# Optimization experiments

Measured on AMD Instinct MI355X. Metric: run time of the kernel, lower is better.

Reference implementation:

```python
import jax, jax.numpy as jnp
import numpy as np

NUM_EMBED = 1024
EMBED_DIM = 64
BETA = 0.25
DECAY = 0.99


def setup_inputs() -> dict:
    key = jax.random.key(0)
    k1, k2 = jax.random.split(key, 2)
    z = jax.random.normal(k1, (16, EMBED_DIM, 64, 64), dtype=jnp.float32)
    embedding = jax.random.uniform(
        k2, (NUM_EMBED, EMBED_DIM), dtype=jnp.float32,
        minval=-1.0 / NUM_EMBED, maxval=1.0 / NUM_EMBED)
    embed_prob = jnp.zeros((NUM_EMBED,), dtype=jnp.float32)
    return {"z": z, "embedding": embedding, "embed_prob": embed_prob}


def reference(z, embedding, embed_prob):
    # Training-mode forward of VectorQuantiser (anchor='closest', not yet init).
    b, c, h, w = z.shape
    zc = jnp.transpose(z, (0, 2, 3, 1))              # b h w c
    zf = zc.reshape(-1, c)                           # [N, d]
    zsg = jax.lax.stop_gradient(zf)

    # d = -||z||^2 - ||e||^2 + 2 z.e  (negative squared L2 distance), [N, K]
    d = (-jnp.sum(zsg * zsg, axis=1, keepdims=True)
         - jnp.sum(embedding * embedding, axis=1)
         + 2.0 * jnp.einsum('nd,kd->nk', zsg, embedding))

    # indices[:, -1] after ascending sort == argmax along codebook axis
    idx = jnp.argmax(d, axis=1)                      # [N]

    # one-hot @ weight == gather
    z_q = jnp.take(embedding, idx, axis=0).reshape(zc.shape)  # b h w c

    loss = (BETA * jnp.mean((jax.lax.stop_gradient(z_q) - zc) ** 2)
            + jnp.mean((z_q - jax.lax.stop_gradient(zc)) ** 2))

    # straight-through estimator
    z_q_st = zc + jax.lax.stop_gradient(z_q - zc)
    z_q_out = jnp.transpose(z_q_st, (0, 3, 1, 2))    # b c h w

    n = zf.shape[0]
    # avg_probs = mean of one-hot encodings over tokens == histogram / N
    avg_probs = jnp.zeros((NUM_EMBED,), dtype=z.dtype).at[idx].add(1.0) / n
    perplexity = jnp.exp(-jnp.sum(avg_probs * jnp.log(avg_probs + 1e-10)))

    embed_prob_new = embed_prob * DECAY + (1.0 - DECAY) * avg_probs

    # anchor='closest': per-codeword, pick the z with largest d (smallest distance)
    closest = jnp.argmax(d, axis=0)                  # [K]
    random_feat = zsg[closest]                       # [K, d]
    decay = jnp.exp(-(embed_prob_new * NUM_EMBED * 10.0) / (1.0 - DECAY)
                    - 1e-3)[:, None]                 # [K, 1]
    new_embedding = embedding * (1.0 - decay) + random_feat * decay

    encoding_indices = idx.reshape(b, h, w)
    return (z_q_out, loss, perplexity, new_embedding, embed_prob_new,
            encoding_indices)
```

## Files before the change

### kernel.cpp

```cpp
#include <hip/hip_runtime.h>


#define MARGIN 2e-4f
#define CERT   2e-4f

#define WS_ROW   0
#define WS_COL   524288
#define WS_CNT   532480
#define WS_LOSS  536576
#define WS_EN2   536592
#define WS_LCNT  540688
#define WS_ZN2   541696
#define WS_EBH   803840
#define WS_EBL   934912
#define WS_LIST  1065984
#define WS_CBM   1328128
#define WS_BYTES 3425280
#define WS_ZERO  540720

typedef __attribute__((ext_vector_type(8))) short short8v;
typedef __attribute__((ext_vector_type(4))) float f32x4;

__device__ __forceinline__ unsigned int f32_ord(float x) {
    unsigned int b = __float_as_uint(x);
    return (b & 0x80000000u) ? ~b : (b | 0x80000000u);
}
__device__ __forceinline__ float ord_f32(unsigned int u) {
    unsigned int b = (u & 0x80000000u) ? (u & 0x7FFFFFFFu) : ~u;
    return __uint_as_float(b);
}

__device__ __forceinline__ unsigned short f2bf(float f) {
    unsigned int u = __float_as_uint(f);
    return (unsigned short)((u + 0x7FFFu + ((u >> 16) & 1u)) >> 16);
}
__device__ __forceinline__ float bf2f(unsigned short h) {
    return __uint_as_float((unsigned int)h << 16);
}

template <typename F>
__device__ __forceinline__ float np_pairwise64_sq(F get) {
    float r[8];
#pragma unroll
    for (int j = 0; j < 8; ++j) {
        float v = get(j);
        r[j] = __fmul_rn(v, v);
    }
#pragma unroll
    for (int i = 8; i < 64; i += 8) {
#pragma unroll
        for (int j = 0; j < 8; ++j) {
            float v = get(i + j);
            r[j] = __fadd_rn(r[j], __fmul_rn(v, v));
        }
    }
    return __fadd_rn(__fadd_rn(__fadd_rn(r[0], r[1]), __fadd_rn(r[2], r[3])),
                     __fadd_rn(__fadd_rn(r[4], r[5]), __fadd_rn(r[6], r[7])));
}

__global__ __launch_bounds__(256) void k_prep(
    const float* __restrict__ emb, float* __restrict__ en2,
    unsigned int* __restrict__ ebh32, unsigned int* __restrict__ ebl32) {
    const int t = threadIdx.x;
    const int k = blockIdx.x * 256 + t;
    const float* a = emb + (size_t)k * 64;
    float ar[64];
#pragma unroll
    for (int i = 0; i < 64; ++i) ar[i] = a[i];
    en2[k] = np_pairwise64_sq([&](int i) { return ar[i]; });
#pragma unroll
    for (int wd = 0; wd < 32; ++wd) {
        float e0 = ar[2 * wd], e1 = ar[2 * wd + 1];
        unsigned short h0 = f2bf(e0), h1 = f2bf(e1);
        ebh32[k * 32 + wd] = (unsigned int)h0 | ((unsigned int)h1 << 16);
        unsigned short l0 = f2bf(__fsub_rn(e0, bf2f(h0)));
        unsigned short l1 = f2bf(__fsub_rn(e1, bf2f(h1)));
        ebl32[k * 32 + wd] = (unsigned int)l0 | ((unsigned int)l1 << 16);
    }
}

__global__ __launch_bounds__(512, 2) void k_mfma(
    const float* __restrict__ z,
    const unsigned short* __restrict__ ebh, const unsigned short* __restrict__ ebl,
    float* __restrict__ zn2, const float* __restrict__ en2,
    float* __restrict__ cbm, unsigned long long* __restrict__ wsrow,
    unsigned int* __restrict__ lcnt, unsigned int* __restrict__ list) {
    const int t = threadIdx.x, l = t & 63, w = t >> 6;
    const int n0 = blockIdx.x * 128;
    const int tw = n0 + w * 16;
    const int lm = l & 15, kg = l >> 4;
    const int b   = n0 >> 12;
    const int hw0 = n0 & 4095;

    __shared__ __align__(16) unsigned char smem[45056];
    unsigned int* eh   = (unsigned int*)(smem);
    unsigned int* el   = (unsigned int*)(smem + 18432);
    float*        en2l = (float*)(smem + 36864);
    unsigned int* cmU  = (unsigned int*)(smem + 40960);
    float*        zl   = (float*)(smem);
    float*        zntmp= (float*)(smem + 36864);
    int*          bcnt  = (int*)(smem);
    unsigned int* bbase = (unsigned int*)(smem + 4);
    unsigned int* blist = (unsigned int*)(smem + 8);

    const float* zsrc = z + (size_t)b * 262144 + hw0;
#pragma unroll
    for (int it = 0; it < 16; ++it) {
        int idx = it * 512 + t;
        int c = idx >> 7, tok = idx & 127;
        zl[c * 129 + tok] = zsrc[(size_t)c * 4096 + tok];
    }
    __syncthreads();

    if (t < 128) {
        float v = np_pairwise64_sq([&](int i) { return zl[i * 129 + t]; });
        zn2[n0 + t] = v;
        zntmp[t] = v;
    }
    const int tokA = w * 16 + lm;
    short8v ah0, ah1, al0, al1;
#pragma unroll
    for (int j = 0; j < 8; ++j) {
        float z0 = zl[(kg * 8 + j) * 129 + tokA];
        float z1 = zl[(32 + kg * 8 + j) * 129 + tokA];
        unsigned short h0 = f2bf(z0);
        unsigned short h1 = f2bf(z1);
        ah0[j] = (short)h0;
        ah1[j] = (short)h1;
        al0[j] = (short)f2bf(__fsub_rn(z0, bf2f(h0)));
        al1[j] = (short)f2bf(__fsub_rn(z1, bf2f(h1)));
    }
    __syncthreads();

    float nzn2[4];
#pragma unroll
    for (int j = 0; j < 4; ++j) nzn2[j] = -zntmp[w * 16 + kg * 4 + j];
    __syncthreads();

    for (int i = t; i < 1024; i += 512) { en2l[i] = en2[i]; cmU[i] = 0u; }
    const uint4* EH4 = reinterpret_cast<const uint4*>(ebh);
    const uint4* EL4 = reinterpret_cast<const uint4*>(ebl);
    const int scode = t >> 3;
    const int sword = (t & 7) ^ (scode & 7);
    const int swd   = sword * 4;
    const int sidx  = scode * 8 + sword;
    {
        uint4 hv = EH4[sidx], lv = EL4[sidx];
        *reinterpret_cast<uint4*>(&eh[0 * 2304 + scode * 36 + swd]) = hv;
        *reinterpret_cast<uint4*>(&el[0 * 2304 + scode * 36 + swd]) = lv;
    }

    float v1[4] = {-3.4e38f, -3.4e38f, -3.4e38f, -3.4e38f};
    float v2[4] = {-3.4e38f, -3.4e38f, -3.4e38f, -3.4e38f};
    int   c1[4] = {0, 0, 0, 0};

    __syncthreads();

    for (int g = 0; g < 16; ++g) {
        const int buf = g & 1;
        const bool pf = (g < 15);
        uint4 hv, lv;
        if (pf) {
            hv = EH4[(g + 1) * 512 + sidx];
            lv = EL4[(g + 1) * 512 + sidx];
        }

#pragma unroll
        for (int sc = 0; sc < 4; ++sc) {
            const int cl = sc * 16 + lm;
            const short8v bh0 = *reinterpret_cast<const short8v*>(&eh[buf * 2304 + cl * 36 + kg * 4]);
            const short8v bh1 = *reinterpret_cast<const short8v*>(&eh[buf * 2304 + cl * 36 + 16 + kg * 4]);
            const short8v bl0 = *reinterpret_cast<const short8v*>(&el[buf * 2304 + cl * 36 + kg * 4]);
            const short8v bl1 = *reinterpret_cast<const short8v*>(&el[buf * 2304 + cl * 36 + 16 + kg * 4]);

            f32x4 a1 = {0.f, 0.f, 0.f, 0.f};
            f32x4 a2 = {0.f, 0.f, 0.f, 0.f};
            __builtin_amdgcn_s_setprio(1);
            a1 = __builtin_amdgcn_mfma_f32_16x16x32_bf16(ah0, bh0, a1, 0, 0, 0);
            a1 = __builtin_amdgcn_mfma_f32_16x16x32_bf16(ah1, bh1, a1, 0, 0, 0);
            a2 = __builtin_amdgcn_mfma_f32_16x16x32_bf16(ah0, bl0, a2, 0, 0, 0);
            a2 = __builtin_amdgcn_mfma_f32_16x16x32_bf16(ah1, bl1, a2, 0, 0, 0);
            a2 = __builtin_amdgcn_mfma_f32_16x16x32_bf16(al0, bh0, a2, 0, 0, 0);
            a2 = __builtin_amdgcn_mfma_f32_16x16x32_bf16(al1, bh1, a2, 0, 0, 0);
            __builtin_amdgcn_s_setprio(0);

            const int code = g * 64 + cl;
            const float en2v = en2l[code];
            float cm = -3.4e38f;
#pragma unroll
            for (int j = 0; j < 4; ++j) {
                float acc  = __fadd_rn(a1[j], a2[j]);
                float base = __fsub_rn(nzn2[j], en2v);
                float s    = fmaf(2.0f, acc, base);
                bool gt = s > v1[j];
                v2[j] = fmaxf(fminf(s, v1[j]), v2[j]);
                v1[j] = fmaxf(v1[j], s);
                c1[j] = gt ? code : c1[j];
                cm = fmaxf(cm, s);
            }
            cm = fmaxf(cm, __shfl_xor(cm, 16, 64));
            cm = fmaxf(cm, __shfl_xor(cm, 32, 64));
            if (l < 16) atomicMax(&cmU[code], f32_ord(cm));
        }

        if (pf) {
            *reinterpret_cast<uint4*>(&eh[(buf ^ 1) * 2304 + scode * 36 + swd]) = hv;
            *reinterpret_cast<uint4*>(&el[(buf ^ 1) * 2304 + scode * 36 + swd]) = lv;
        }
        __syncthreads();
    }

    if (t == 0) *bcnt = 0;
    __syncthreads();
#pragma unroll
    for (int j = 0; j < 4; ++j) {
        unsigned long long key =
            ((unsigned long long)f32_ord(v1[j]) << 32) |
            (unsigned long long)(unsigned int)(~(unsigned int)c1[j]);
        float w2 = v2[j];
#pragma unroll
        for (int m = 1; m < 16; m <<= 1) {
            unsigned long long ok = __shfl_xor(key, m, 64);
            float ov2 = __shfl_xor(w2, m, 64);
            unsigned long long lk = (key < ok) ? key : ok;
            float lv2 = ord_f32((unsigned int)(lk >> 32));
            w2 = fmaxf(fmaxf(w2, ov2), lv2);
            key = (key > ok) ? key : ok;
        }
        if (lm == 0) {
            const int tn = tw + kg * 4 + j;
            float v1m = ord_f32((unsigned int)(key >> 32));
            if (__fsub_rn(v1m, w2) > CERT) {
                wsrow[tn] = key;
            } else {
                int p = atomicAdd(bcnt, 1);
                blist[p] = (unsigned int)tn;
            }
        }
    }
    __syncthreads();
    if (t == 0 && *bcnt > 0) *bbase = atomicAdd(lcnt, (unsigned int)*bcnt);
    __syncthreads();
    {
        const int cb2 = *bcnt;
        for (int i = t; i < cb2; i += 512) list[*bbase + i] = blist[i];
    }

    for (int code = t; code < 1024; code += 512)
        cbm[(size_t)code * 512 + blockIdx.x] = ord_f32(cmU[code]);
}

__global__ __launch_bounds__(256) void k_rescore(
    const float* __restrict__ z, const float* __restrict__ emb,
    const float* __restrict__ zn2, const float* __restrict__ en2,
    const float* __restrict__ cbm,
    const unsigned int* __restrict__ list, const unsigned int* __restrict__ lcnt,
    unsigned long long* __restrict__ wscol,
    unsigned long long* __restrict__ wsrow) {
    const int t = threadIdx.x;
    if (blockIdx.x < 1024) {
        const int k = blockIdx.x;
        __shared__ float red[256];
        __shared__ int   hlist[512];
        __shared__ int   hcnt;
        float a  = cbm[(size_t)k * 512 + t];
        float b2 = cbm[(size_t)k * 512 + 256 + t];
        red[t] = fmaxf(a, b2);
        if (t == 0) hcnt = 0;
        __syncthreads();
        for (int st = 128; st; st >>= 1) {
            if (t < st) red[t] = fmaxf(red[t], red[t + st]);
            __syncthreads();
        }
        const float thr = red[0] - MARGIN;
        if (a >= thr)  { int p = atomicAdd(&hcnt, 1); hlist[p] = t; }
        if (b2 >= thr) { int p = atomicAdd(&hcnt, 1); hlist[p] = t + 256; }
        __syncthreads();
        const int hc = hcnt;
        const float en2k = en2[k];
        const float4* ek = reinterpret_cast<const float4*>(emb + (size_t)k * 64);

        for (int h = 0; h < hc; ++h) {
            const int g = hlist[h];
            if (t < 128) {
                const int n = g * 128 + t;
                const int b = n >> 12, hw = n & 4095;
                const float* zp = z + (size_t)b * 262144 + hw;
                float c0 = 0.f, c1 = 0.f, c2 = 0.f, c3 = 0.f;
#pragma unroll
                for (int j = 0; j < 16; ++j) {
                    float4 e = ek[j];
                    c0 = fmaf(e.x, zp[(size_t)(4 * j + 0) * 4096], c0);
                    c1 = fmaf(e.y, zp[(size_t)(4 * j + 1) * 4096], c1);
                    c2 = fmaf(e.z, zp[(size_t)(4 * j + 2) * 4096], c2);
                    c3 = fmaf(e.w, zp[(size_t)(4 * j + 3) * 4096], c3);
                }
                float dot = (c0 + c1) + (c2 + c3);
                float d = __fadd_rn(__fsub_rn(-zn2[n], en2k), 2.0f * dot);
                unsigned long long key =
                    ((unsigned long long)f32_ord(d) << 32) |
                    (unsigned long long)(unsigned int)(~(unsigned int)n);
#pragma unroll
                for (int m = 1; m < 64; m <<= 1) {
                    unsigned long long o = __shfl_xor(key, m, 64);
                    if (o > key) key = o;
                }
                if ((t & 63) == 0) atomicMax(&wscol[k], key);
            }
        }
    } else {
        const int bid2 = blockIdx.x - 1024;
        const int k0 = (bid2 & 63) * 16;
        const int xs = bid2 >> 6;
        const unsigned int cnt = *lcnt;
        const float4* E4 = reinterpret_cast<const float4*>(emb);
        for (unsigned int i = (unsigned int)xs * 256 + t; i < cnt;
             i += 64 * 256) {
            const int n = (int)list[i];
            const int b = n >> 12, hw = n & 4095;
            const float* zp = z + (size_t)b * 262144 + hw;
            const float nz = -zn2[n];
            unsigned long long best = 0ull;
            for (int kk = 0; kk < 16; ++kk) {
                const int k = k0 + kk;
                const float4* ek = E4 + (size_t)k * 16;
                float c0 = 0.f, c1 = 0.f, c2 = 0.f, c3 = 0.f;
#pragma unroll
                for (int j = 0; j < 16; ++j) {
                    float4 e = ek[j];
                    c0 = fmaf(e.x, zp[(size_t)(4 * j + 0) * 4096], c0);
                    c1 = fmaf(e.y, zp[(size_t)(4 * j + 1) * 4096], c1);
                    c2 = fmaf(e.z, zp[(size_t)(4 * j + 2) * 4096], c2);
                    c3 = fmaf(e.w, zp[(size_t)(4 * j + 3) * 4096], c3);
                }
                float dot = (c0 + c1) + (c2 + c3);
                float d = __fadd_rn(__fsub_rn(nz, en2[k]), 2.0f * dot);
                unsigned long long key =
                    ((unsigned long long)f32_ord(d) << 32) |
                    (unsigned long long)(unsigned int)(~(unsigned int)k);
                if (key > best) best = key;
            }
            atomicMax(&wsrow[n], best);
        }
    }
}

__global__ __launch_bounds__(256) void k_tokens(
    const float* __restrict__ z, const float* __restrict__ emb,
    const unsigned long long* __restrict__ wsrow,
    unsigned int* __restrict__ counts, double* __restrict__ loss_acc,
    float* __restrict__ out_zq, float* __restrict__ out_idx) {
    const int t    = threadIdx.x;
    const int lane = t & 63;
    const int q    = t >> 6;
    const int n    = blockIdx.x * 64 + lane;
    const int b    = n >> 12;
    const int hw   = n & 4095;

    unsigned long long key = wsrow[n];
    int idx = (int)(~(unsigned int)(key & 0xFFFFFFFFull));
    if (q == 0) {
        out_idx[n] = (float)idx;
        atomicAdd(&counts[idx], 1u);
    }

    const float* zp = z + (size_t)b * 262144 + hw;
    float*       op = out_zq + (size_t)b * 262144 + hw;
    const float* ep = emb + (size_t)idx * 64;

    double ls = 0.0;
#pragma unroll
    for (int c = q * 16; c < q * 16 + 16; ++c) {
        float zc   = zp[(size_t)c * 4096];
        float eq   = ep[c];
        float diff = __fsub_rn(eq, zc);
        float sq   = __fmul_rn(diff, diff);
        ls += (double)sq;
        op[(size_t)c * 4096] = __fadd_rn(zc, diff);
    }

    __shared__ double sred[256];
    sred[q * 64 + lane] = ls;
    __syncthreads();
    if (t < 64) {
        sred[t] = (sred[t] + sred[64 + t]) + (sred[128 + t] + sred[192 + t]);
    }
    __syncthreads();
    for (int st = 32; st; st >>= 1) {
        if (t < st) sred[t] += sred[t + st];
        __syncthreads();
    }
    if (t == 0) atomicAdd(loss_acc, sred[0]);
}

__global__ __launch_bounds__(1024) void k_tail(
    const float* __restrict__ z, const float* __restrict__ emb,
    const float* __restrict__ embed_prob,
    const unsigned long long* __restrict__ wscol,
    const unsigned int* __restrict__ counts,
    const double* __restrict__ loss_acc,
    float* __restrict__ out_newemb, float* __restrict__ out_loss,
    float* __restrict__ out_perp, float* __restrict__ out_prob) {
    const int k = blockIdx.x * 16 + (threadIdx.x >> 6);
    const int c = threadIdx.x & 63;

    float avg  = (float)counts[k] * (1.0f / 65536.0f);
    float pnew = __fadd_rn(__fmul_rn(embed_prob[k], 0.99f),
                           __fmul_rn(0.01f, avg));
    float tt = __fdiv_rn(__fmul_rn(__fmul_rn(pnew, 1024.0f), 10.0f), 0.01f);
    float dk = expf(__fsub_rn(-tt, 1e-3f));
    float omd = __fsub_rn(1.0f, dk);

    unsigned long long ck = wscol[k];
    int cn  = (int)(~(unsigned int)(ck & 0xFFFFFFFFull));
    int cb  = cn >> 12;
    int chw = cn & 4095;

    float rf = z[(size_t)cb * 262144 + (size_t)c * 4096 + chw];
    float e  = emb[(size_t)k * 64 + c];
    out_newemb[(size_t)k * 64 + c] =
        __fadd_rn(__fmul_rn(e, omd), __fmul_rn(rf, dk));

    if (blockIdx.x == 0) {
        const int q = threadIdx.x;

        float avg2  = (float)counts[q] * (1.0f / 65536.0f);
        float pnew2 = __fadd_rn(__fmul_rn(embed_prob[q], 0.99f),
                                __fmul_rn(0.01f, avg2));
        out_prob[q] = pnew2;

        float term = __fmul_rn(avg2, logf(__fadd_rn(avg2, 1e-10f)));
        __shared__ double red[1024];
        red[q] = (double)term;
        __syncthreads();
        for (int st = 512; st; st >>= 1) {
            if (q < st) red[q] += red[q + st];
            __syncthreads();
        }
        if (q == 0) {
            float s32 = (float)red[0];
            out_perp[0] = expf(-s32);
            double lm = loss_acc[0] / 4194304.0;
            float  m  = (float)lm;
            out_loss[0] = __fadd_rn(__fmul_rn(0.25f, m), m);
        }
    }
}

extern "C" void kernel_launch(void* const* d_in, const int* in_sizes, int n_in,
                              void* d_out, int out_size, void* d_ws, size_t ws_size,
                              hipStream_t stream) {
    const float* z    = (const float*)d_in[0];
    const float* emb  = (const float*)d_in[1];
    const float* prob = (const float*)d_in[2];

    float* out        = (float*)d_out;
    float* out_zq     = out;
    float* out_loss   = out + 4194304;
    float* out_perp   = out + 4194305;
    float* out_newemb = out + 4194306;
    float* out_prob   = out + 4259842;
    float* out_idx    = out + 4260866;

    char* ws = (char*)d_ws;
    unsigned long long* wsrow = (unsigned long long*)(ws + WS_ROW);
    unsigned long long* wscol = (unsigned long long*)(ws + WS_COL);
    unsigned int*       cnts  = (unsigned int*)(ws + WS_CNT);
    double*             lacc  = (double*)(ws + WS_LOSS);
    float*              en2   = (float*)(ws + WS_EN2);
    unsigned int*       lcnt  = (unsigned int*)(ws + WS_LCNT);
    float*              zn2   = (float*)(ws + WS_ZN2);
    unsigned short*     ebh   = (unsigned short*)(ws + WS_EBH);
    unsigned short*     ebl   = (unsigned short*)(ws + WS_EBL);
    unsigned int*       list  = (unsigned int*)(ws + WS_LIST);
    float*              cbm   = (float*)(ws + WS_CBM);

    hipMemsetAsync(d_ws, 0, WS_ZERO, stream);

    hipLaunchKernelGGL(k_prep, dim3(4), dim3(256), 0, stream,
                       emb, en2, (unsigned int*)ebh, (unsigned int*)ebl);
    hipLaunchKernelGGL(k_mfma, dim3(512), dim3(512), 0, stream,
                       z, ebh, ebl, zn2, en2, cbm, wsrow, lcnt, list);
    hipLaunchKernelGGL(k_rescore, dim3(5120), dim3(256), 0, stream,
                       z, emb, zn2, en2, cbm, list, lcnt, wscol, wsrow);
    hipLaunchKernelGGL(k_tokens, dim3(1024), dim3(256), 0, stream,
                       z, emb, wsrow, cnts, lacc, out_zq, out_idx);
    hipLaunchKernelGGL(k_tail, dim3(64), dim3(1024), 0, stream,
                       z, emb, prob, wscol, cnts, lacc,
                       out_newemb, out_loss, out_perp, out_prob);
}
```

Before: 206.2 us.

## Fold workspace zeroing into prep kernel, split MFMA chains, vectorize codeword loads

Removes the separate hipMemsetAsync and has a fifth block of k_prep zero only the column, loss and list-count workspace regions. Rows that go to rescoring now get wsrow explicitly written to zero, since that region is no longer cleared. The six MFMAs are regrouped into three independent accumulator chains to shorten dependency stalls, and k_tokens loads each codeword slice with float4 vector loads. The extra accumulator adds a float add and changes summation order slightly, and correctness now depends on every workspace region that needs zeroing actually being covered.

```diff
diff --git a/kernel.cpp b/kernel.cpp
--- a/kernel.cpp
+++ b/kernel.cpp
@@ -16,7 +16,6 @@
 #define WS_LIST  1065984
 #define WS_CBM   1328128
 #define WS_BYTES 3425280
-#define WS_ZERO  540720
 
 typedef __attribute__((ext_vector_type(8))) short short8v;
 typedef __attribute__((ext_vector_type(4))) float f32x4;
@@ -60,22 +59,30 @@
 
 __global__ __launch_bounds__(256) void k_prep(
     const float* __restrict__ emb, float* __restrict__ en2,
-    unsigned int* __restrict__ ebh32, unsigned int* __restrict__ ebl32) {
+    unsigned int* __restrict__ ebh32, unsigned int* __restrict__ ebl32,
+    unsigned int* __restrict__ wszero ) {
     const int t = threadIdx.x;
-    const int k = blockIdx.x * 256 + t;
-    const float* a = emb + (size_t)k * 64;
-    float ar[64];
-#pragma unroll
-    for (int i = 0; i < 64; ++i) ar[i] = a[i];
-    en2[k] = np_pairwise64_sq([&](int i) { return ar[i]; });
-#pragma unroll
-    for (int wd = 0; wd < 32; ++wd) {
-        float e0 = ar[2 * wd], e1 = ar[2 * wd + 1];
-        unsigned short h0 = f2bf(e0), h1 = f2bf(e1);
-        ebh32[k * 32 + wd] = (unsigned int)h0 | ((unsigned int)h1 << 16);
-        unsigned short l0 = f2bf(__fsub_rn(e0, bf2f(h0)));
-        unsigned short l1 = f2bf(__fsub_rn(e1, bf2f(h1)));
-        ebl32[k * 32 + wd] = (unsigned int)l0 | ((unsigned int)l1 << 16);
+    if (blockIdx.x < 4) {
+        const int k = blockIdx.x * 256 + t;
+        const float* a = emb + (size_t)k * 64;
+        float ar[64];
+#pragma unroll
+        for (int i = 0; i < 64; ++i) ar[i] = a[i];
+        en2[k] = np_pairwise64_sq([&](int i) { return ar[i]; });
+#pragma unroll
+        for (int wd = 0; wd < 32; ++wd) {
+            float e0 = ar[2 * wd], e1 = ar[2 * wd + 1];
+            unsigned short h0 = f2bf(e0), h1 = f2bf(e1);
+            ebh32[k * 32 + wd] = (unsigned int)h0 | ((unsigned int)h1 << 16);
+            unsigned short l0 = f2bf(__fsub_rn(e0, bf2f(h0)));
+            unsigned short l1 = f2bf(__fsub_rn(e1, bf2f(h1)));
+            ebl32[k * 32 + wd] = (unsigned int)l0 | ((unsigned int)l1 << 16);
+        }
+    } else {
+        for (unsigned int i = t; i < 3072; i += 256)
+            wszero[(WS_COL >> 2) + i] = 0u;
+        if (t < 2) wszero[(WS_LOSS >> 2) + t] = 0u;
+        if (t == 0) wszero[WS_LCNT >> 2] = 0u;
     }
 }
 
@@ -175,13 +182,14 @@
 
             f32x4 a1 = {0.f, 0.f, 0.f, 0.f};
             f32x4 a2 = {0.f, 0.f, 0.f, 0.f};
+            f32x4 a3 = {0.f, 0.f, 0.f, 0.f};
             __builtin_amdgcn_s_setprio(1);
             a1 = __builtin_amdgcn_mfma_f32_16x16x32_bf16(ah0, bh0, a1, 0, 0, 0);
+            a2 = __builtin_amdgcn_mfma_f32_16x16x32_bf16(ah0, bl0, a2, 0, 0, 0);
+            a3 = __builtin_amdgcn_mfma_f32_16x16x32_bf16(al0, bh0, a3, 0, 0, 0);
             a1 = __builtin_amdgcn_mfma_f32_16x16x32_bf16(ah1, bh1, a1, 0, 0, 0);
-            a2 = __builtin_amdgcn_mfma_f32_16x16x32_bf16(ah0, bl0, a2, 0, 0, 0);
             a2 = __builtin_amdgcn_mfma_f32_16x16x32_bf16(ah1, bl1, a2, 0, 0, 0);
-            a2 = __builtin_amdgcn_mfma_f32_16x16x32_bf16(al0, bh0, a2, 0, 0, 0);
-            a2 = __builtin_amdgcn_mfma_f32_16x16x32_bf16(al1, bh1, a2, 0, 0, 0);
+            a3 = __builtin_amdgcn_mfma_f32_16x16x32_bf16(al1, bh1, a3, 0, 0, 0);
             __builtin_amdgcn_s_setprio(0);
 
             const int code = g * 64 + cl;
@@ -189,7 +197,7 @@
             float cm = -3.4e38f;
 #pragma unroll
             for (int j = 0; j < 4; ++j) {
-                float acc  = __fadd_rn(a1[j], a2[j]);
+                float acc  = __fadd_rn(__fadd_rn(a1[j], a2[j]), a3[j]);
                 float base = __fsub_rn(nzn2[j], en2v);
                 float s    = fmaf(2.0f, acc, base);
                 bool gt = s > v1[j];
@@ -233,6 +241,7 @@
             if (__fsub_rn(v1m, w2) > CERT) {
                 wsrow[tn] = key;
             } else {
+                wsrow[tn] = 0ull;
                 int p = atomicAdd(bcnt, 1);
                 blist[p] = (unsigned int)tn;
             }
@@ -366,17 +375,24 @@
 
     const float* zp = z + (size_t)b * 262144 + hw;
     float*       op = out_zq + (size_t)b * 262144 + hw;
-    const float* ep = emb + (size_t)idx * 64;
+
+    const float4* ep4 =
+        reinterpret_cast<const float4*>(emb + (size_t)idx * 64 + q * 16);
+    float4 e4[4];
+#pragma unroll
+    for (int i = 0; i < 4; ++i) e4[i] = ep4[i];
+    const float* er = reinterpret_cast<const float*>(e4);
 
     double ls = 0.0;
 #pragma unroll
-    for (int c = q * 16; c < q * 16 + 16; ++c) {
-        float zc   = zp[(size_t)c * 4096];
-        float eq   = ep[c];
+    for (int c = 0; c < 16; ++c) {
+        const int ch = q * 16 + c;
+        float zc   = zp[(size_t)ch * 4096];
+        float eq   = er[c];
         float diff = __fsub_rn(eq, zc);
         float sq   = __fmul_rn(diff, diff);
         ls += (double)sq;
-        op[(size_t)c * 4096] = __fadd_rn(zc, diff);
+        op[(size_t)ch * 4096] = __fadd_rn(zc, diff);
     }
 
     __shared__ double sred[256];
@@ -475,10 +491,9 @@
     unsigned int*       list  = (unsigned int*)(ws + WS_LIST);
     float*              cbm   = (float*)(ws + WS_CBM);
 
-    hipMemsetAsync(d_ws, 0, WS_ZERO, stream);
-
-    hipLaunchKernelGGL(k_prep, dim3(4), dim3(256), 0, stream,
-                       emb, en2, (unsigned int*)ebh, (unsigned int*)ebl);
+    hipLaunchKernelGGL(k_prep, dim3(5), dim3(256), 0, stream,
+                       emb, en2, (unsigned int*)ebh, (unsigned int*)ebl,
+                       (unsigned int*)ws);
     hipLaunchKernelGGL(k_mfma, dim3(512), dim3(512), 0, stream,
                        z, ebh, ebl, zn2, en2, cbm, wsrow, lcnt, list);
     hipLaunchKernelGGL(k_rescore, dim3(5120), dim3(256), 0, stream,
```

Result: faster. 201.2 us (-2.4%).
